# Kernel tuning notes

Hardware: AMD Instinct MI355X
Metric: run time of the kernel (lower is better)

The kernel has to match this reference:

```python
import jax, jax.numpy as jnp
import numpy as np

D_MODEL = 2048
N_HEADS = 16
HEAD_DIM = D_MODEL // N_HEADS  # 128
B, S = 2, 2048


def setup_inputs() -> dict:
    key = jax.random.key(0)
    k1, k2, k3, k4 = jax.random.split(key, 4)
    scale = 0.02
    X = jax.random.normal(k1, (B, S, D_MODEL), dtype=jnp.float32)
    Wq = jax.random.normal(k2, (D_MODEL, D_MODEL), dtype=jnp.float32) * scale
    Wkv = jax.random.normal(k3, (2 * HEAD_DIM, D_MODEL), dtype=jnp.float32) * scale
    Wo = jax.random.normal(k4, (D_MODEL, D_MODEL), dtype=jnp.float32) * scale
    return {"X": X, "Wq": Wq, "Wkv": Wkv, "Wo": Wo}


def reference(X, Wq, Wkv, Wo):
    Bt, St, Dm = X.shape
    # Q: [B, H, S, hd]
    Q = (X @ Wq.T).reshape(Bt, St, N_HEADS, HEAD_DIM).transpose(0, 2, 1, 3)
    # Shared single-head K/V: [B, S, hd] each (no materialized head broadcast)
    KV = X @ Wkv.T
    K, V = KV[..., :HEAD_DIM], KV[..., HEAD_DIM:]
    # Scores: [B, H, S, S]; K shared across heads via einsum broadcast
    scores = jnp.einsum("bhqd,bkd->bhqk", Q, K) / jnp.sqrt(jnp.float32(HEAD_DIM))
    causal = jnp.tril(jnp.ones((St, St), dtype=bool))
    scores = jnp.where(causal[None, None], scores, jnp.finfo(scores.dtype).min)
    attn = jax.nn.softmax(scores, axis=-1)
    heads = jnp.einsum("bhqk,bkd->bhqd", attn, V)  # [B, H, S, hd]
    concat = heads.transpose(0, 2, 1, 3).reshape(Bt, St, Dm)
    return concat @ Wo.T
```

## Files before the change

kernel.cpp:

```cpp
#include <hip/hip_runtime.h>
#include <hip/hip_bf16.h>
#include <stdint.h>

#define DM 2048
#define NH 16
#define HD 128
#define NB 2
#define SQ 2048

typedef __bf16 bf16x8 __attribute__((ext_vector_type(8)));
typedef float f32x4 __attribute__((ext_vector_type(4)));

typedef __attribute__((address_space(1))) uint32_t as1_u32;
typedef __attribute__((address_space(3))) uint32_t as3_u32;

__device__ __forceinline__ void gload16(const void* g, void* l) {
  __builtin_amdgcn_global_load_lds((const as1_u32*)g, (as3_u32*)l, 16, 0, 0);
}

__device__ __forceinline__ unsigned short f2bf(float f) {
  __hip_bfloat16 h = __float2bfloat16(f);
  return __builtin_bit_cast(unsigned short, h);
}

__global__ void cast_f32_to_bf16(const float* __restrict__ in,
                                 unsigned short* __restrict__ out, int n) {
  int stride = gridDim.x * blockDim.x * 4;
  for (int i = (blockIdx.x * blockDim.x + threadIdx.x) * 4; i < n; i += stride) {
    float4 v = *reinterpret_cast<const float4*>(in + i);
    ushort4 o;
    o.x = f2bf(v.x); o.y = f2bf(v.y); o.z = f2bf(v.z); o.w = f2bf(v.w);
    *reinterpret_cast<ushort4*>(out + i) = o;
  }
}

template<int MODE>
__global__ void gemm_bt(const unsigned short* __restrict__ A,
                        const unsigned short* __restrict__ Bm,
                        void* __restrict__ C0, void* __restrict__ C1,
                        int M, int N, int K, float scale) {
  __shared__ unsigned short As[128 * 32];
  __shared__ unsigned short Bs[128 * 32];
  const int t = threadIdx.x;
  const int w = t >> 6, l = t & 63;
  const int lr = l & 15, lkb = (l >> 4) * 8;
  const int m0 = blockIdx.x * 128, n0 = blockIdx.y * 128;
  const int wr = (w >> 1) * 64, wc = (w & 1) * 64;
  f32x4 acc[4][4] = {};
  for (int k0 = 0; k0 < K; k0 += 32) {
#pragma unroll
    for (int p = 0; p < 2; ++p) {
      int seg = p * 256 + t;
      int row = seg >> 2, c8 = (seg & 3) * 8;
      gload16(A + (size_t)(m0 + row) * K + k0 + c8, (void*)(As + seg * 8));
      gload16(Bm + (size_t)(n0 + row) * K + k0 + c8, (void*)(Bs + seg * 8));
    }
    __syncthreads();
    bf16x8 af[4], bfv[4];
#pragma unroll
    for (int mi = 0; mi < 4; ++mi)
      af[mi] = *reinterpret_cast<const bf16x8*>(As + (wr + mi * 16 + lr) * 32 + lkb);
#pragma unroll
    for (int ni = 0; ni < 4; ++ni)
      bfv[ni] = *reinterpret_cast<const bf16x8*>(Bs + (wc + ni * 16 + lr) * 32 + lkb);
#pragma unroll
    for (int mi = 0; mi < 4; ++mi)
#pragma unroll
      for (int ni = 0; ni < 4; ++ni)
        acc[mi][ni] = __builtin_amdgcn_mfma_f32_16x16x32_bf16(af[mi], bfv[ni], acc[mi][ni], 0, 0, 0);
    __syncthreads();
  }
#pragma unroll
  for (int mi = 0; mi < 4; ++mi) {
#pragma unroll
    for (int ni = 0; ni < 4; ++ni) {
      const int r0 = m0 + wr + mi * 16 + (l >> 4) * 4;
      const int cc = n0 + wc + ni * 16 + lr;
#pragma unroll
      for (int j = 0; j < 4; ++j) {
        float v = acc[mi][ni][j];
        if (MODE == 0) {
          ((unsigned short*)C0)[(size_t)(r0 + j) * N + cc] = f2bf(v * scale);
        } else if (MODE == 1) {
          ((float*)C0)[(size_t)(r0 + j) * N + cc] = v;
        } else {
          int m = r0 + j;
          unsigned short hv = f2bf(v);
          if (cc < HD) {
            ((unsigned short*)C0)[(size_t)m * HD + cc] = hv;
          } else {
            int b = m >> 11, s = m & (SQ - 1);
            ((unsigned short*)C1)[((size_t)b * HD + (cc - HD)) * SQ + s] = hv;
          }
        }
      }
    }
  }
}

__global__ __launch_bounds__(256) void mqa_attn(const unsigned short* __restrict__ Qb,
                                                const unsigned short* __restrict__ Kc,
                                                const unsigned short* __restrict__ Vt,
                                                unsigned short* __restrict__ Hb) {
  __shared__ unsigned short Ks[128 * 128];
  __shared__ unsigned short Vs[128 * 128];
  const int t = threadIdx.x, w = t >> 6, l = t & 63;
  const int lr = l & 15, hi = l >> 4;
  const int lkb = hi * 8;
  const int x7 = lr & 7;
  const int id = blockIdx.x;
  const int pp = id & 255;
  const int bh = pp >> 3, k8 = pp & 7;
  const int qt = (id < 256) ? (15 - k8) : k8;
  const int b = bh >> 4, h = bh & 15;
  const int q0 = qt * 128;

  bf16x8 qf[2][4];
#pragma unroll
  for (int mi = 0; mi < 2; ++mi)
#pragma unroll
    for (int kk = 0; kk < 4; ++kk) {
      const uint4* p = reinterpret_cast<const uint4*>(
          Qb + (size_t)(b * SQ + q0 + w * 32 + mi * 16 + lr) * DM + h * HD + kk * 32 + lkb);
      qf[mi][kk] = __builtin_bit_cast(bf16x8, *p);
    }
  f32x4 o[2][8] = {};
  float mrun[2][4], lrun[2][4];
#pragma unroll
  for (int mi = 0; mi < 2; ++mi)
#pragma unroll
    for (int j = 0; j < 4; ++j) { mrun[mi][j] = -3.0e38f; lrun[mi][j] = 0.f; }

  for (int kt = 0; kt <= qt; ++kt) {
    const unsigned short* Kg = Kc + (size_t)(b * SQ + kt * 128) * HD;
    const unsigned short* Vg = Vt + (size_t)b * HD * SQ + kt * 128;
#pragma unroll
    for (int p = 0; p < 8; ++p) {
      int seg = p * 256 + t;
      int row = seg >> 4, sl = seg & 15;
      int slx = sl ^ (row & 7);
      gload16(Kg + (size_t)row * HD + slx * 8, (void*)(Ks + seg * 8));
      gload16(Vg + (size_t)row * SQ + slx * 8, (void*)(Vs + seg * 8));
    }
    __syncthreads();

    f32x4 s[2][8] = {};
#pragma unroll
    for (int kk = 0; kk < 4; ++kk) {
      bf16x8 kf[8];
#pragma unroll
      for (int ni = 0; ni < 8; ++ni)
        kf[ni] = *reinterpret_cast<const bf16x8*>(
            Ks + (ni * 16 + lr) * 128 + (((kk * 4 + hi) ^ x7) << 3));
#pragma unroll
      for (int mi = 0; mi < 2; ++mi)
#pragma unroll
        for (int ni = 0; ni < 8; ++ni)
          s[mi][ni] = __builtin_amdgcn_mfma_f32_16x16x32_bf16(qf[mi][kk], kf[ni], s[mi][ni], 0, 0, 0);
    }

    if (kt == qt) {
#pragma unroll
      for (int mi = 0; mi < 2; ++mi)
#pragma unroll
        for (int ni = 0; ni < 8; ++ni)
#pragma unroll
          for (int j = 0; j < 4; ++j) {
            int rq = w * 32 + mi * 16 + hi * 4 + j;
            int ck = ni * 16 + lr;
            if (ck > rq) s[mi][ni][j] = -3.0e38f;
          }
    }

#pragma unroll
    for (int mi = 0; mi < 2; ++mi) {
#pragma unroll
      for (int j = 0; j < 4; ++j) {
        float pm = s[mi][0][j];
#pragma unroll
        for (int ni = 1; ni < 8; ++ni) pm = fmaxf(pm, s[mi][ni][j]);
#pragma unroll
        for (int dd = 1; dd < 16; dd <<= 1) pm = fmaxf(pm, __shfl_xor(pm, dd));
        float mnew = fmaxf(mrun[mi][j], pm);
        float sc = __expf(mrun[mi][j] - mnew);
        mrun[mi][j] = mnew;
        float rs = 0.f;
#pragma unroll
        for (int ni = 0; ni < 8; ++ni) {
          float pv = __expf(s[mi][ni][j] - mnew);
          s[mi][ni][j] = pv;
          rs += pv;
        }
#pragma unroll
        for (int dd = 1; dd < 16; dd <<= 1) rs += __shfl_xor(rs, dd);
        lrun[mi][j] = lrun[mi][j] * sc + rs;
#pragma unroll
        for (int ni = 0; ni < 8; ++ni) o[mi][ni][j] *= sc;
      }
    }

    __syncthreads();
    unsigned short* Ps = Ks + w * 32 * 128;
#pragma unroll
    for (int mi = 0; mi < 2; ++mi)
#pragma unroll
      for (int ni = 0; ni < 8; ++ni)
#pragma unroll
        for (int j = 0; j < 4; ++j) {
          int prow = mi * 16 + hi * 4 + j;
          int psl = (ni * 2 + (lr >> 3)) ^ (prow & 7);
          Ps[prow * 128 + psl * 8 + (lr & 7)] = f2bf(s[mi][ni][j]);
        }

#pragma unroll
    for (int kk = 0; kk < 4; ++kk) {
      bf16x8 pa[2], vf[8];
#pragma unroll
      for (int mi = 0; mi < 2; ++mi)
        pa[mi] = *reinterpret_cast<const bf16x8*>(
            Ps + (mi * 16 + lr) * 128 + (((kk * 4 + hi) ^ x7) << 3));
#pragma unroll
      for (int ni = 0; ni < 8; ++ni)
        vf[ni] = *reinterpret_cast<const bf16x8*>(
            Vs + (ni * 16 + lr) * 128 + (((kk * 4 + hi) ^ x7) << 3));
#pragma unroll
      for (int mi = 0; mi < 2; ++mi)
#pragma unroll
        for (int ni = 0; ni < 8; ++ni)
          o[mi][ni] = __builtin_amdgcn_mfma_f32_16x16x32_bf16(pa[mi], vf[ni], o[mi][ni], 0, 0, 0);
    }
    __syncthreads();
  }

#pragma unroll
  for (int mi = 0; mi < 2; ++mi)
#pragma unroll
    for (int ni = 0; ni < 8; ++ni)
#pragma unroll
      for (int j = 0; j < 4; ++j) {
        int q = q0 + w * 32 + mi * 16 + hi * 4 + j;
        float val = o[mi][ni][j] / lrun[mi][j];
        Hb[(size_t)(b * SQ + q) * DM + h * HD + ni * 16 + lr] = f2bf(val);
      }
}

extern "C" void kernel_launch(void* const* d_in, const int* in_sizes, int n_in,
                              void* d_out, int out_size, void* d_ws, size_t ws_size,
                              hipStream_t stream) {
  const float* X   = (const float*)d_in[0];
  const float* Wq  = (const float*)d_in[1];
  const float* Wkv = (const float*)d_in[2];
  const float* Wo  = (const float*)d_in[3];
  char* ws = (char*)d_ws;
  unsigned short* Xb   = (unsigned short*)(ws + 0);
  unsigned short* Wqb  = (unsigned short*)(ws + 16777216);
  unsigned short* Wob  = (unsigned short*)(ws + 25165824);
  unsigned short* Wkvb = (unsigned short*)(ws + 33554432);
  unsigned short* Qb   = (unsigned short*)(ws + 34603008);
  unsigned short* Kc   = (unsigned short*)(ws + 51380224);
  unsigned short* Vt   = (unsigned short*)(ws + 52428800);
  unsigned short* Hb   = (unsigned short*)(ws + 53477376);

  cast_f32_to_bf16<<<2048, 256, 0, stream>>>(X, Xb, NB * SQ * DM);
  cast_f32_to_bf16<<<1024, 256, 0, stream>>>(Wq, Wqb, DM * DM);
  cast_f32_to_bf16<<<512, 256, 0, stream>>>(Wkv, Wkvb, 2 * HD * DM);
  cast_f32_to_bf16<<<1024, 256, 0, stream>>>(Wo, Wob, DM * DM);

  gemm_bt<0><<<dim3(32, 16), 256, 0, stream>>>(Xb, Wqb, Qb, nullptr,
                                               NB * SQ, DM, DM, 0.08838834764831845f);
  gemm_bt<2><<<dim3(32, 2), 256, 0, stream>>>(Xb, Wkvb, Kc, Vt,
                                              NB * SQ, 2 * HD, DM, 1.0f);
  mqa_attn<<<512, 256, 0, stream>>>(Qb, Kc, Vt, Hb);
  gemm_bt<1><<<dim3(32, 16), 256, 0, stream>>>(Hb, Wob, d_out, nullptr,
                                               NB * SQ, DM, DM, 1.0f);
}
```

Baseline: 348.3 us.

## Fuse QKV projection and weight casts, vectorize P stores with permuted V layout

The three weight-cast kernels become one launch, and the Q and KV projections become one GEMM over a concatenated Wq|Wkv weight (N=2304). Its epilogue routes output columns to Q (scaled), K, or a key-permuted transposed V. In attention, the LDS XOR swizzle changes to mix higher row bits. The P tile is now written with one 16-byte store per row instead of scalar stores, using a column permutation that the V layout matches. The online-softmax rescale of O and l now runs only when the row max grows, at the cost of extra index arithmetic and a data-dependent branch.

```diff
diff --git a/kernel.cpp b/kernel.cpp
--- a/kernel.cpp
+++ b/kernel.cpp
@@ -22,6 +22,8 @@
   __hip_bfloat16 h = __float2bfloat16(f);
   return __builtin_bit_cast(unsigned short, h);
 }
+
+__device__ __forceinline__ int swz(int r) { return (r ^ (r >> 3)) & 7; }
 
 __global__ void cast_f32_to_bf16(const float* __restrict__ in,
                                  unsigned short* __restrict__ out, int n) {
@@ -34,10 +36,30 @@
   }
 }
 
+__global__ void cast_weights(const float* __restrict__ Wq,
+                             const float* __restrict__ Wkv,
+                             const float* __restrict__ Wo,
+                             unsigned short* __restrict__ Wqkvb,
+                             unsigned short* __restrict__ Wob) {
+  const int n = 4194304 + 524288 + 4194304;
+  int stride = gridDim.x * blockDim.x * 4;
+  for (int i = (blockIdx.x * blockDim.x + threadIdx.x) * 4; i < n; i += stride) {
+    const float* src; unsigned short* dst;
+    if (i < 4194304)      { src = Wq + i;            dst = Wqkvb + i; }
+    else if (i < 4718592) { src = Wkv + (i - 4194304); dst = Wqkvb + i; }
+    else                  { src = Wo + (i - 4718592);  dst = Wob + (i - 4718592); }
+    float4 v = *reinterpret_cast<const float4*>(src);
+    ushort4 o;
+    o.x = f2bf(v.x); o.y = f2bf(v.y); o.z = f2bf(v.z); o.w = f2bf(v.w);
+    *reinterpret_cast<ushort4*>(dst) = o;
+  }
+}
+
 template<int MODE>
 __global__ void gemm_bt(const unsigned short* __restrict__ A,
                         const unsigned short* __restrict__ Bm,
                         void* __restrict__ C0, void* __restrict__ C1,
+                        void* __restrict__ C2,
                         int M, int N, int K, float scale) {
   __shared__ unsigned short As[128 * 32];
   __shared__ unsigned short Bs[128 * 32];
@@ -79,18 +101,19 @@
 #pragma unroll
       for (int j = 0; j < 4; ++j) {
         float v = acc[mi][ni][j];
-        if (MODE == 0) {
-          ((unsigned short*)C0)[(size_t)(r0 + j) * N + cc] = f2bf(v * scale);
-        } else if (MODE == 1) {
+        if (MODE == 1) {
           ((float*)C0)[(size_t)(r0 + j) * N + cc] = v;
         } else {
           int m = r0 + j;
-          unsigned short hv = f2bf(v);
-          if (cc < HD) {
-            ((unsigned short*)C0)[(size_t)m * HD + cc] = hv;
+          if (cc < DM) {
+            ((unsigned short*)C0)[(size_t)m * DM + cc] = f2bf(v * scale);
+          } else if (cc < DM + HD) {
+            ((unsigned short*)C1)[(size_t)m * HD + (cc - DM)] = f2bf(v);
           } else {
             int b = m >> 11, s = m & (SQ - 1);
-            ((unsigned short*)C1)[((size_t)b * HD + (cc - HD)) * SQ + s] = hv;
+            int c = s & 127;
+            int sp = (s & ~127) + ((c & 15) * 8 + (c >> 4));
+            ((unsigned short*)C2)[((size_t)b * HD + (cc - DM - HD)) * SQ + sp] = f2bf(v);
           }
         }
       }
@@ -107,7 +130,6 @@
   const int t = threadIdx.x, w = t >> 6, l = t & 63;
   const int lr = l & 15, hi = l >> 4;
   const int lkb = hi * 8;
-  const int x7 = lr & 7;
   const int id = blockIdx.x;
   const int pp = id & 255;
   const int bh = pp >> 3, k8 = pp & 7;
@@ -138,7 +160,7 @@
     for (int p = 0; p < 8; ++p) {
       int seg = p * 256 + t;
       int row = seg >> 4, sl = seg & 15;
-      int slx = sl ^ (row & 7);
+      int slx = sl ^ swz(row);
       gload16(Kg + (size_t)row * HD + slx * 8, (void*)(Ks + seg * 8));
       gload16(Vg + (size_t)row * SQ + slx * 8, (void*)(Vs + seg * 8));
     }
@@ -149,9 +171,11 @@
     for (int kk = 0; kk < 4; ++kk) {
       bf16x8 kf[8];
 #pragma unroll
-      for (int ni = 0; ni < 8; ++ni)
+      for (int ni = 0; ni < 8; ++ni) {
+        int r = ni * 16 + lr;
         kf[ni] = *reinterpret_cast<const bf16x8*>(
-            Ks + (ni * 16 + lr) * 128 + (((kk * 4 + hi) ^ x7) << 3));
+            Ks + r * 128 + (((kk * 4 + hi) ^ swz(r)) << 3));
+      }
 #pragma unroll
       for (int mi = 0; mi < 2; ++mi)
 #pragma unroll
@@ -181,9 +205,14 @@
         for (int ni = 1; ni < 8; ++ni) pm = fmaxf(pm, s[mi][ni][j]);
 #pragma unroll
         for (int dd = 1; dd < 16; dd <<= 1) pm = fmaxf(pm, __shfl_xor(pm, dd));
-        float mnew = fmaxf(mrun[mi][j], pm);
-        float sc = __expf(mrun[mi][j] - mnew);
-        mrun[mi][j] = mnew;
+        if (pm > mrun[mi][j]) {
+          float sc = __expf(mrun[mi][j] - pm);
+          mrun[mi][j] = pm;
+          lrun[mi][j] *= sc;
+#pragma unroll
+          for (int ni = 0; ni < 8; ++ni) o[mi][ni][j] *= sc;
+        }
+        float mnew = mrun[mi][j];
         float rs = 0.f;
 #pragma unroll
         for (int ni = 0; ni < 8; ++ni) {
@@ -193,9 +222,7 @@
         }
 #pragma unroll
         for (int dd = 1; dd < 16; dd <<= 1) rs += __shfl_xor(rs, dd);
-        lrun[mi][j] = lrun[mi][j] * sc + rs;
-#pragma unroll
-        for (int ni = 0; ni < 8; ++ni) o[mi][ni][j] *= sc;
+        lrun[mi][j] += rs;
       }
     }
 
@@ -204,25 +231,30 @@
 #pragma unroll
     for (int mi = 0; mi < 2; ++mi)
 #pragma unroll
-      for (int ni = 0; ni < 8; ++ni)
-#pragma unroll
-        for (int j = 0; j < 4; ++j) {
-          int prow = mi * 16 + hi * 4 + j;
-          int psl = (ni * 2 + (lr >> 3)) ^ (prow & 7);
-          Ps[prow * 128 + psl * 8 + (lr & 7)] = f2bf(s[mi][ni][j]);
-        }
+      for (int j = 0; j < 4; ++j) {
+        int prow = mi * 16 + hi * 4 + j;
+        unsigned short pk[8];
+#pragma unroll
+        for (int ni = 0; ni < 8; ++ni) pk[ni] = f2bf(s[mi][ni][j]);
+        *reinterpret_cast<uint4*>(Ps + prow * 128 + ((lr ^ swz(prow)) << 3)) =
+            *reinterpret_cast<const uint4*>(pk);
+      }
 
 #pragma unroll
     for (int kk = 0; kk < 4; ++kk) {
       bf16x8 pa[2], vf[8];
 #pragma unroll
-      for (int mi = 0; mi < 2; ++mi)
+      for (int mi = 0; mi < 2; ++mi) {
+        int r = mi * 16 + lr;
         pa[mi] = *reinterpret_cast<const bf16x8*>(
-            Ps + (mi * 16 + lr) * 128 + (((kk * 4 + hi) ^ x7) << 3));
-#pragma unroll
-      for (int ni = 0; ni < 8; ++ni)
+            Ps + r * 128 + (((kk * 4 + hi) ^ swz(r)) << 3));
+      }
+#pragma unroll
+      for (int ni = 0; ni < 8; ++ni) {
+        int r = ni * 16 + lr;
         vf[ni] = *reinterpret_cast<const bf16x8*>(
-            Vs + (ni * 16 + lr) * 128 + (((kk * 4 + hi) ^ x7) << 3));
+            Vs + r * 128 + (((kk * 4 + hi) ^ swz(r)) << 3));
+      }
 #pragma unroll
       for (int mi = 0; mi < 2; ++mi)
 #pragma unroll
@@ -252,25 +284,21 @@
   const float* Wkv = (const float*)d_in[2];
   const float* Wo  = (const float*)d_in[3];
   char* ws = (char*)d_ws;
-  unsigned short* Xb   = (unsigned short*)(ws + 0);
-  unsigned short* Wqb  = (unsigned short*)(ws + 16777216);
-  unsigned short* Wob  = (unsigned short*)(ws + 25165824);
-  unsigned short* Wkvb = (unsigned short*)(ws + 33554432);
-  unsigned short* Qb   = (unsigned short*)(ws + 34603008);
-  unsigned short* Kc   = (unsigned short*)(ws + 51380224);
-  unsigned short* Vt   = (unsigned short*)(ws + 52428800);
-  unsigned short* Hb   = (unsigned short*)(ws + 53477376);
+  unsigned short* Xb    = (unsigned short*)(ws + 0);
+  unsigned short* Wqkvb = (unsigned short*)(ws + 16777216);
+  unsigned short* Wob   = (unsigned short*)(ws + 26214400);
+  unsigned short* Qb    = (unsigned short*)(ws + 34603008);
+  unsigned short* Kc    = (unsigned short*)(ws + 51380224);
+  unsigned short* Vt    = (unsigned short*)(ws + 52428800);
+  unsigned short* Hb    = (unsigned short*)(ws + 53477376);
 
   cast_f32_to_bf16<<<2048, 256, 0, stream>>>(X, Xb, NB * SQ * DM);
-  cast_f32_to_bf16<<<1024, 256, 0, stream>>>(Wq, Wqb, DM * DM);
-  cast_f32_to_bf16<<<512, 256, 0, stream>>>(Wkv, Wkvb, 2 * HD * DM);
-  cast_f32_to_bf16<<<1024, 256, 0, stream>>>(Wo, Wob, DM * DM);
-
-  gemm_bt<0><<<dim3(32, 16), 256, 0, stream>>>(Xb, Wqb, Qb, nullptr,
-                                               NB * SQ, DM, DM, 0.08838834764831845f);
-  gemm_bt<2><<<dim3(32, 2), 256, 0, stream>>>(Xb, Wkvb, Kc, Vt,
-                                              NB * SQ, 2 * HD, DM, 1.0f);
+  cast_weights<<<2048, 256, 0, stream>>>(Wq, Wkv, Wo, Wqkvb, Wob);
+
+  gemm_bt<2><<<dim3(32, 18), 256, 0, stream>>>(Xb, Wqkvb, Qb, Kc, Vt,
+                                               NB * SQ, DM + 2 * HD, DM,
+                                               0.08838834764831845f);
   mqa_attn<<<512, 256, 0, stream>>>(Qb, Kc, Vt, Hb);
-  gemm_bt<1><<<dim3(32, 16), 256, 0, stream>>>(Hb, Wob, d_out, nullptr,
+  gemm_bt<1><<<dim3(32, 16), 256, 0, stream>>>(Hb, Wob, d_out, nullptr, nullptr,
                                                NB * SQ, DM, DM, 1.0f);
 }
```

Result: faster. 314.3 us (-9.8%).
